# Optimization experiments

Measured on AMD Instinct MI355X. Metric: run time of the kernel, lower is better.

Reference implementation:

```python
import jax, jax.numpy as jnp
import numpy as np

B, T, HE, L, HD = 512, 512, 512, 64, 512

def setup_inputs() -> dict:
    key = jax.random.key(0)
    ks = jax.random.split(key, 16)
    def w(k, shape):
        return jax.random.normal(k, shape, dtype=jnp.float32) * 0.05
    z32 = lambda n: jnp.zeros((n,), jnp.float32)
    return {
        "input_tensor": jax.random.normal(ks[0], (B, T, 1), dtype=jnp.float32),
        # encoder LSTMCell (keras gate order i, f, g, o)
        "enc_W": w(ks[1], (1, 4 * HE)),
        "enc_U": w(ks[2], (HE, 4 * HE)),
        "enc_b": z32(4 * HE),
        # encoder mu / std heads
        "emu_W": w(ks[3], (HE, L)), "emu_b": z32(L),
        "estd_W": w(ks[4], (HE, L)), "estd_b": z32(L),
        # decoder first-state dense (tanh)
        "dfs_W": w(ks[5], (L, HD)), "dfs_b": z32(HD),
        # decoder LSTMCell
        "dec_W": w(ks[6], (L, 4 * HD)),
        "dec_U": w(ks[7], (HD, 4 * HD)),
        "dec_b": z32(4 * HD),
        # decoder mu / std heads (Dense(1))
        "dmu_W": w(ks[8], (HD, 1)), "dmu_b": z32(1),
        "dstd_W": w(ks[9], (HD, 1)), "dstd_b": z32(1),
    }

def _lstm_update(gates, c):
    i, f, g, o = jnp.split(gates, 4, axis=-1)
    c_new = jax.nn.sigmoid(f) * c + jax.nn.sigmoid(i) * jnp.tanh(g)
    h_new = jax.nn.sigmoid(o) * jnp.tanh(c_new)
    return h_new, c_new

def reference(input_tensor, enc_W, enc_U, enc_b, emu_W, emu_b, estd_W, estd_b,
              dfs_W, dfs_b, dec_W, dec_U, dec_b, dmu_W, dmu_b, dstd_W, dstd_b):
    x = input_tensor
    Bn, Tn = x.shape[0], x.shape[1]
    He = enc_U.shape[0]

    # ---- encoder: LSTM over time, keep final h ----
    def enc_step(carry, xt):
        h, c = carry
        gates = xt @ enc_W + h @ enc_U + enc_b
        return _lstm_update(gates, c), None
    h0 = jnp.zeros((Bn, He), x.dtype)
    (hT, _), _ = jax.lax.scan(enc_step, (h0, h0), jnp.swapaxes(x, 0, 1))

    mu_enc = hT @ emu_W + emu_b                       # [B, L]
    sigma_enc = jax.nn.softplus(hT @ estd_W + estd_b)  # [B, L]
    z = mu_enc  # call() uses reparam=False -> latent returns mu

    # ---- decoder: LSTM fed constant z each step ----
    hd = jnp.tanh(z @ dfs_W + dfs_b)                  # [B, HD]
    cd = jnp.zeros_like(hd)
    zin = z @ dec_W + dec_b                           # input projection constant over t
    def dec_step(carry, _):
        h, c = carry
        h_new, c_new = _lstm_update(zin + h @ dec_U, c)
        mu = h_new @ dmu_W + dmu_b                    # [B, 1]
        sg = h_new @ dstd_W + dstd_b
        return (h_new, c_new), (mu, sg)
    _, (mus, sgs) = jax.lax.scan(dec_step, (hd, cd), None, length=Tn)

    mu_dec = jnp.swapaxes(mus, 0, 1)                  # [B, T, 1]
    sigma_dec = jax.nn.softplus(jnp.swapaxes(sgs, 0, 1))
    return (mu_dec, sigma_dec, mu_enc, sigma_enc)
```

## Files before the change

### kernel.cpp

```cpp
#include <hip/hip_runtime.h>


#define B_ 512
#define T_ 512
#define H_ 512

typedef _Float16 f16;
typedef _Float16 f16x8 __attribute__((ext_vector_type(8)));
typedef float f32x16 __attribute__((ext_vector_type(16)));
typedef unsigned long long u64;
typedef unsigned int u32;

#define OFF_SG_DEC 262144
#define OFF_MU_ENC 524288
#define OFF_SG_ENC 557056

__device__ __forceinline__ float sigm_(float x) { return 1.f / (1.f + __expf(-x)); }
__device__ __forceinline__ float tanh_(float x) {
  float t = fabsf(x);
  float e = __expf(2.f * t);
  float r = 1.f - 2.f / (e + 1.f);
  return x < 0.f ? -r : r;
}
__device__ __forceinline__ float softplus_(float x) {
  return fmaxf(x, 0.f) + log1pf(__expf(-fabsf(x)));
}
__device__ __forceinline__ int fresh_(u64 w, u32 g) {
  return ((u32)(w >> 48) == g) & (((u32)(w >> 16) & 0xffffu) == g);
}
__device__ __forceinline__ u32 packh_(u64 w) {
  return (u32)(w & 0xffffu) | (((u32)(w >> 32) & 0xffffu) << 16);
}

__global__ void pack_U(const float* __restrict__ U, f16* __restrict__ Upk) {
  const int e = blockIdx.x * 256 + threadIdx.x;
  const int j = e & 7, lane = (e >> 3) & 63, ks = (e >> 9) & 31;
  const int w = (e >> 14) & 7, wg = (e >> 17) & 7;
  const int ccol = lane & 31, khalf = lane >> 5;
  const int uu = ccol >> 2, gate = ccol & 3;
  const int k = ks * 16 + khalf * 8 + j;
  const int gcol = gate * 512 + wg * 64 + w * 8 + uu;
  Upk[e] = (f16)U[k * 2048 + gcol];
}

template <int IS_DEC>
__global__ void __launch_bounds__(512, 1)
lstm_rec(const f16* __restrict__ Upk,
         const float* __restrict__ xin,
         const float* __restrict__ wa,
         const float* __restrict__ wb,
         u32* __restrict__ hbuf,
         float* __restrict__ accmu,
         float* __restrict__ accsg) {
  const int bid = blockIdx.x;
  const int s = bid >> 3;
  const int j = (bid & 7) * 4 + (s & 3);
  const int wg = s >> 2;
  const int tid = threadIdx.x, wave = tid >> 6, lane = tid & 63;
  const int U0 = wg * 64;
  const int RA = j * 16, RB = j * 16 + 8;
  const u32 GB = IS_DEC ? 0x8000u : 0u;
  const int ccol = lane & 31, khalf = lane >> 5;

  f16x8 Breg[32];
#pragma unroll
  for (int ks = 0; ks < 32; ++ks) {
    const f16* p = Upk + (((wg * 8 + wave) * 32 + ks) << 9) + lane * 8;
    asm volatile("global_load_dwordx4 %0, %1, off\n\ts_waitcnt vmcnt(0)"
                 : "=v"(Breg[ks]) : "v"(p));
  }

  const int erow = tid >> 6, eu = tid & 63;
  float xwv[4], bias[4], addA[4], addB[4];
  float dmu_w = 0.f, dstd_w = 0.f;
#pragma unroll
  for (int gt = 0; gt < 4; ++gt) {
    const int col = gt * 512 + U0 + eu;
    if (IS_DEC) {
      addA[gt] = xin[(RA + erow) * 2048 + col];
      addB[gt] = xin[(RB + erow) * 2048 + col];
      xwv[gt] = 0.f; bias[gt] = 0.f;
    } else {
      bias[gt] = wb[col];
      xwv[gt] = wa[col];
      addA[gt] = 0.f; addB[gt] = 0.f;
    }
  }
  if (IS_DEC) { dmu_w = wa[U0 + eu]; dstd_w = wb[U0 + eu]; }

  float cA = 0.f, cB = 0.f;

  __shared__ __align__(16) f16 bufA[8 * 520];
  __shared__ __align__(16) f16 bufB[8 * 520];
  __shared__ __align__(16) float gatesL[8 * 264];

  int lrow[4], lcol[4], gidxA[4], gidxB[4];
#pragma unroll
  for (int i = 0; i < 4; ++i) {
    const int w = tid + i * 512;
    lrow[i] = w >> 8; lcol[i] = w & 255;
    gidxA[i] = (RA + lrow[i]) * 256 + lcol[i];
    gidxB[i] = (RB + lrow[i]) * 256 + lcol[i];
  }
  const u64* hb64 = (const u64*)hbuf;

  u64 wAr[4], wBr[4];
#pragma unroll
  for (int i = 0; i < 4; ++i)
    wAr[i] = __hip_atomic_load(hb64 + gidxA[i], __ATOMIC_RELAXED,
                               __HIP_MEMORY_SCOPE_AGENT);
  asm volatile("" ::: "memory");

  for (int t = 0; t < T_; ++t) {
    const int b0 = (t & 1) * 131072;
    const int b1 = ((t + 1) & 1) * 131072;
    const int c1 = ((t + 1) & 1) * 262144;
    const u32 gr = GB + (u32)t, gn = GB + (u32)t + 1u;

    while (!(fresh_(wAr[0], gr) & fresh_(wAr[1], gr) &
             fresh_(wAr[2], gr) & fresh_(wAr[3], gr))) {
#pragma unroll
      for (int i = 0; i < 4; ++i)
        wAr[i] = __hip_atomic_load(hb64 + b0 + gidxA[i], __ATOMIC_RELAXED,
                                   __HIP_MEMORY_SCOPE_AGENT);
    }
#pragma unroll
    for (int i = 0; i < 4; ++i)
      *(u32*)&bufA[lrow[i] * 520 + lcol[i] * 2] = packh_(wAr[i]);
    __syncthreads();

#pragma unroll
    for (int i = 0; i < 4; ++i)
      wBr[i] = __hip_atomic_load(hb64 + b0 + gidxB[i], __ATOMIC_RELAXED,
                                 __HIP_MEMORY_SCOPE_AGENT);
    asm volatile("" ::: "memory");

    {
      f32x16 acc;
#pragma unroll
      for (int q = 0; q < 16; ++q) acc[q] = 0.f;
#pragma unroll
      for (int ks = 0; ks < 32; ++ks) {
        f16x8 a = *(const f16x8*)&bufA[(lane & 7) * 520 + ks * 16 + khalf * 8];
        acc = __builtin_amdgcn_mfma_f32_32x32x16_f16(a, Breg[ks], acc, 0, 0, 0);
      }
#pragma unroll
      for (int r = 0; r < 4; ++r)
        gatesL[(r + 4 * khalf) * 264 + wave * 32 + ccol] = acc[r];
    }
    __syncthreads();

    {
      const float4 g4 = *(const float4*)&gatesL[erow * 264 + (eu >> 3) * 32 + (eu & 7) * 4];
      float ga0, ga1, ga2, ga3;
      if (IS_DEC) {
        ga0 = g4.x + addA[0]; ga1 = g4.y + addA[1];
        ga2 = g4.z + addA[2]; ga3 = g4.w + addA[3];
      } else {
        const float xv = xin[(RA + erow) * T_ + t];
        ga0 = g4.x + bias[0] + xv * xwv[0];
        ga1 = g4.y + bias[1] + xv * xwv[1];
        ga2 = g4.z + bias[2] + xv * xwv[2];
        ga3 = g4.w + bias[3] + xv * xwv[3];
      }
      const float cn = sigm_(ga1) * cA + sigm_(ga0) * tanh_(ga2);
      cA = cn;
      const float hn = sigm_(ga3) * tanh_(cn);
      union { f16 h; unsigned short u; } hc; hc.h = (f16)hn;
      __hip_atomic_store(hbuf + c1 + (RA + erow) * 512 + U0 + eu,
                         (gn << 16) | (u32)hc.u, __ATOMIC_RELAXED,
                         __HIP_MEMORY_SCOPE_AGENT);
      if (IS_DEC) {
        float smu = hn * dmu_w, ssg = hn * dstd_w;
#pragma unroll
        for (int o = 32; o; o >>= 1) {
          smu += __shfl_xor(smu, o);
          ssg += __shfl_xor(ssg, o);
        }
        if (lane == 0) {
          unsafeAtomicAdd(&accmu[(RA + erow) * T_ + t], smu);
          unsafeAtomicAdd(&accsg[(RA + erow) * T_ + t], ssg);
        }
      }
    }

    while (!(fresh_(wBr[0], gr) & fresh_(wBr[1], gr) &
             fresh_(wBr[2], gr) & fresh_(wBr[3], gr))) {
#pragma unroll
      for (int i = 0; i < 4; ++i)
        wBr[i] = __hip_atomic_load(hb64 + b0 + gidxB[i], __ATOMIC_RELAXED,
                                   __HIP_MEMORY_SCOPE_AGENT);
    }
#pragma unroll
    for (int i = 0; i < 4; ++i)
      *(u32*)&bufB[lrow[i] * 520 + lcol[i] * 2] = packh_(wBr[i]);
    __syncthreads();

#pragma unroll
    for (int i = 0; i < 4; ++i)
      wAr[i] = __hip_atomic_load(hb64 + b1 + gidxA[i], __ATOMIC_RELAXED,
                                 __HIP_MEMORY_SCOPE_AGENT);
    asm volatile("" ::: "memory");

    {
      f32x16 acc;
#pragma unroll
      for (int q = 0; q < 16; ++q) acc[q] = 0.f;
#pragma unroll
      for (int ks = 0; ks < 32; ++ks) {
        f16x8 a = *(const f16x8*)&bufB[(lane & 7) * 520 + ks * 16 + khalf * 8];
        acc = __builtin_amdgcn_mfma_f32_32x32x16_f16(a, Breg[ks], acc, 0, 0, 0);
      }
#pragma unroll
      for (int r = 0; r < 4; ++r)
        gatesL[(r + 4 * khalf) * 264 + wave * 32 + ccol] = acc[r];
    }
    __syncthreads();

    {
      const float4 g4 = *(const float4*)&gatesL[erow * 264 + (eu >> 3) * 32 + (eu & 7) * 4];
      float ga0, ga1, ga2, ga3;
      if (IS_DEC) {
        ga0 = g4.x + addB[0]; ga1 = g4.y + addB[1];
        ga2 = g4.z + addB[2]; ga3 = g4.w + addB[3];
      } else {
        const float xv = xin[(RB + erow) * T_ + t];
        ga0 = g4.x + bias[0] + xv * xwv[0];
        ga1 = g4.y + bias[1] + xv * xwv[1];
        ga2 = g4.z + bias[2] + xv * xwv[2];
        ga3 = g4.w + bias[3] + xv * xwv[3];
      }
      const float cn = sigm_(ga1) * cB + sigm_(ga0) * tanh_(ga2);
      cB = cn;
      const float hn = sigm_(ga3) * tanh_(cn);
      union { f16 h; unsigned short u; } hc; hc.h = (f16)hn;
      __hip_atomic_store(hbuf + c1 + (RB + erow) * 512 + U0 + eu,
                         (gn << 16) | (u32)hc.u, __ATOMIC_RELAXED,
                         __HIP_MEMORY_SCOPE_AGENT);
      if (IS_DEC) {
        float smu = hn * dmu_w, ssg = hn * dstd_w;
#pragma unroll
        for (int o = 32; o; o >>= 1) {
          smu += __shfl_xor(smu, o);
          ssg += __shfl_xor(ssg, o);
        }
        if (lane == 0) {
          unsafeAtomicAdd(&accmu[(RB + erow) * T_ + t], smu);
          unsafeAtomicAdd(&accsg[(RB + erow) * T_ + t], ssg);
        }
      }
    }
  }
}

__global__ void enc_heads(const u32* __restrict__ h0, const float* __restrict__ emuW,
                          const float* __restrict__ emub, const float* __restrict__ estdW,
                          const float* __restrict__ estdb, float* __restrict__ out,
                          float* __restrict__ z) {
  const int b = blockIdx.x, tid = threadIdx.x;
  __shared__ float hrow[512];
  for (int k = tid; k < 512; k += 128) {
    union { unsigned short u; f16 h; } c;
    c.u = (unsigned short)(h0[b * 512 + k] & 0xffffu);
    hrow[k] = (float)c.h;
  }
  __syncthreads();
  const int head = tid >> 6, l = tid & 63;
  const float* W = head ? estdW : emuW;
  float a = 0.f;
#pragma unroll 8
  for (int k = 0; k < 512; ++k) a += hrow[k] * W[k * 64 + l];
  if (head == 0) {
    const float v = a + emub[l];
    out[OFF_MU_ENC + b * 64 + l] = v;
    z[b * 64 + l] = v;
  } else {
    out[OFF_SG_ENC + b * 64 + l] = softplus_(a + estdb[l]);
  }
}

__global__ void dec_prep(const float* __restrict__ z, const float* __restrict__ dfsW,
                         const float* __restrict__ dfsb, const float* __restrict__ decW,
                         const float* __restrict__ decb, u32* __restrict__ hbuf,
                         float* __restrict__ zin) {
  const int b = blockIdx.x, tid = threadIdx.x;
  __shared__ float zl[64];
  if (tid < 64) zl[tid] = z[b * 64 + tid];
  __syncthreads();
  for (int c = tid; c < 512; c += 256) {
    float a = dfsb[c];
#pragma unroll
    for (int l = 0; l < 64; ++l) a += zl[l] * dfsW[l * 512 + c];
    union { f16 h; unsigned short u; } hc; hc.h = (f16)tanh_(a);
    hbuf[b * 512 + c] = (0x8000u << 16) | (u32)hc.u;
  }
  for (int c = tid; c < 2048; c += 256) {
    float a = decb[c];
#pragma unroll
    for (int l = 0; l < 64; ++l) a += zl[l] * decW[l * 2048 + c];
    zin[b * 2048 + c] = a;
  }
}

__global__ void finalize_k(const float* __restrict__ accmu, const float* __restrict__ accsg,
                           const float* __restrict__ dmub, const float* __restrict__ dstdb,
                           float* __restrict__ out) {
  const int i = blockIdx.x * 256 + threadIdx.x;
  out[i] = accmu[i] + dmub[0];
  out[OFF_SG_DEC + i] = softplus_(accsg[i] + dstdb[0]);
}

extern "C" void kernel_launch(void* const* d_in, const int* in_sizes, int n_in,
                              void* d_out, int out_size, void* d_ws, size_t ws_size,
                              hipStream_t stream) {
  (void)in_sizes; (void)n_in; (void)out_size; (void)ws_size;
  const float* x     = (const float*)d_in[0];
  const float* encW  = (const float*)d_in[1];
  const float* encU  = (const float*)d_in[2];
  const float* encb  = (const float*)d_in[3];
  const float* emuW  = (const float*)d_in[4];
  const float* emub  = (const float*)d_in[5];
  const float* estdW = (const float*)d_in[6];
  const float* estdb = (const float*)d_in[7];
  const float* dfsW  = (const float*)d_in[8];
  const float* dfsb  = (const float*)d_in[9];
  const float* decW  = (const float*)d_in[10];
  const float* decU  = (const float*)d_in[11];
  const float* decb  = (const float*)d_in[12];
  const float* dmuW  = (const float*)d_in[13];
  const float* dmub  = (const float*)d_in[14];
  const float* dstdW = (const float*)d_in[15];
  const float* dstdb = (const float*)d_in[16];

  char* ws = (char*)d_ws;
  u32*   hbuf  = (u32*)(ws + 0);
  float* accmu = (float*)(ws + (2u << 20));
  float* accsg = (float*)(ws + (3u << 20));
  f16*   UpkE  = (f16*)(ws + (4u << 20));
  float* zin   = (float*)(ws + (4u << 20));
  f16*   UpkD  = (f16*)(ws + (8u << 20));
  float* z     = (float*)(ws + (10u << 20));
  float* out   = (float*)d_out;

  hipMemsetAsync(d_ws, 0, 4u << 20, stream);

  hipLaunchKernelGGL(pack_U, dim3(4096), dim3(256), 0, stream, encU, UpkE);
  hipLaunchKernelGGL(pack_U, dim3(4096), dim3(256), 0, stream, decU, UpkD);

  hipLaunchKernelGGL((lstm_rec<0>), dim3(256), dim3(512), 0, stream,
                     UpkE, x, encW, encb, hbuf, (float*)nullptr, (float*)nullptr);
  hipLaunchKernelGGL(enc_heads, dim3(512), dim3(128), 0, stream,
                     hbuf, emuW, emub, estdW, estdb, out, z);
  hipLaunchKernelGGL(dec_prep, dim3(512), dim3(256), 0, stream,
                     z, dfsW, dfsb, decW, decb, hbuf, zin);
  hipLaunchKernelGGL((lstm_rec<1>), dim3(256), dim3(512), 0, stream,
                     UpkD, zin, dmuW, dstdW, hbuf, accmu, accsg);
  hipLaunchKernelGGL(finalize_k, dim3(1024), dim3(256), 0, stream,
                     accmu, accsg, dmub, dstdb, out);
}
```

Before: 4.916 ms.

## Remove gate LDS round-trip via lane shuffles and compute decoder heads from staged h

The gate LDS staging buffer and its __syncthreads per half-step are replaced by in-register transposition with xor shuffles, so each lane applies the LSTM update directly on MFMA accumulator values. The decoder mu/std head dot products no longer use per-wave atomicAdds on every step. Instead, one workgroup per row group is assigned by rotation to compute them from the previous step's h already staged in LDS, with plain stores. A small tail kernel handles the final timestep, and the memset is shrunk because the accumulators are now fully overwritten. This removes barriers and atomic traffic from the serial recurrence critical path, at the cost of extra shuffles and uneven duty work across workgroups.

```diff
diff --git a/kernel.cpp b/kernel.cpp
--- a/kernel.cpp
+++ b/kernel.cpp
@@ -70,29 +70,36 @@
                  : "=v"(Breg[ks]) : "v"(p));
   }
 
-  const int erow = tid >> 6, eu = tid & 63;
-  float xwv[4], bias[4], addA[4], addB[4];
-  float dmu_w = 0.f, dstd_w = 0.f;
+  const int p_ = ccol & 3, uu_ = ccol >> 2;
+  const int row_l = p_ + 4 * khalf;
+  const int unit_l = wave * 8 + uu_;
+  float biasv[4], xwv[4], addA[4], addB[4];
 #pragma unroll
   for (int gt = 0; gt < 4; ++gt) {
-    const int col = gt * 512 + U0 + eu;
+    const int col = gt * 512 + U0 + unit_l;
     if (IS_DEC) {
-      addA[gt] = xin[(RA + erow) * 2048 + col];
-      addB[gt] = xin[(RB + erow) * 2048 + col];
-      xwv[gt] = 0.f; bias[gt] = 0.f;
+      addA[gt] = xin[(RA + row_l) * 2048 + col];
+      addB[gt] = xin[(RB + row_l) * 2048 + col];
+      biasv[gt] = 0.f; xwv[gt] = 0.f;
     } else {
-      bias[gt] = wb[col];
+      biasv[gt] = wb[col];
       xwv[gt] = wa[col];
       addA[gt] = 0.f; addB[gt] = 0.f;
     }
   }
-  if (IS_DEC) { dmu_w = wa[U0 + eu]; dstd_w = wb[U0 + eu]; }
+  float wmu[8], wsg[8];
+  if (IS_DEC) {
+#pragma unroll
+    for (int q = 0; q < 8; ++q) {
+      wmu[q] = wa[lane * 8 + q];
+      wsg[q] = wb[lane * 8 + q];
+    }
+  }
 
   float cA = 0.f, cB = 0.f;
 
   __shared__ __align__(16) f16 bufA[8 * 520];
   __shared__ __align__(16) f16 bufB[8 * 520];
-  __shared__ __align__(16) float gatesL[8 * 264];
 
   int lrow[4], lcol[4], gidxA[4], gidxB[4];
 #pragma unroll
@@ -116,6 +123,7 @@
     const int b1 = ((t + 1) & 1) * 131072;
     const int c1 = ((t + 1) & 1) * 262144;
     const u32 gr = GB + (u32)t, gn = GB + (u32)t + 1u;
+    const int duty = IS_DEC && t >= 1 && wg == (t & 7);
 
     while (!(fresh_(wAr[0], gr) & fresh_(wAr[1], gr) &
              fresh_(wAr[2], gr) & fresh_(wAr[3], gr))) {
@@ -135,7 +143,27 @@
                                  __HIP_MEMORY_SCOPE_AGENT);
     asm volatile("" ::: "memory");
 
+    if (duty) {
+      const f16x8 hv = *(const f16x8*)&bufA[wave * 520 + lane * 8];
+      float smu = 0.f, ssg = 0.f;
+#pragma unroll
+      for (int q = 0; q < 8; ++q) {
+        const float hq = (float)hv[q];
+        smu += hq * wmu[q]; ssg += hq * wsg[q];
+      }
+#pragma unroll
+      for (int o = 32; o; o >>= 1) {
+        smu += __shfl_xor(smu, o); ssg += __shfl_xor(ssg, o);
+      }
+      if (lane == 0) {
+        accmu[(RA + wave) * 512 + (t - 1)] = smu;
+        accsg[(RA + wave) * 512 + (t - 1)] = ssg;
+      }
+    }
+
     {
+      float xv = 0.f;
+      if (!IS_DEC) xv = xin[(RA + row_l) * T_ + t];
       f32x16 acc;
 #pragma unroll
       for (int q = 0; q < 16; ++q) acc[q] = 0.f;
@@ -144,44 +172,33 @@
         f16x8 a = *(const f16x8*)&bufA[(lane & 7) * 520 + ks * 16 + khalf * 8];
         acc = __builtin_amdgcn_mfma_f32_32x32x16_f16(a, Breg[ks], acc, 0, 0, 0);
       }
-#pragma unroll
-      for (int r = 0; r < 4; ++r)
-        gatesL[(r + 4 * khalf) * 264 + wave * 32 + ccol] = acc[r];
-    }
-    __syncthreads();
-
-    {
-      const float4 g4 = *(const float4*)&gatesL[erow * 264 + (eu >> 3) * 32 + (eu & 7) * 4];
+      const float x0 = acc[0], x1 = acc[1], x2 = acc[2], x3 = acc[3];
+      const int odd1 = lane & 1, odd2 = lane & 2;
+      const float t0 = __shfl_xor(x1, 1), t1 = __shfl_xor(x0, 1);
+      const float t2 = __shfl_xor(x3, 1), t3 = __shfl_xor(x2, 1);
+      const float y0 = odd1 ? t0 : x0, y1 = odd1 ? x1 : t1;
+      const float y2 = odd1 ? t2 : x2, y3 = odd1 ? x3 : t3;
+      const float s0 = __shfl_xor(y2, 2), s1 = __shfl_xor(y3, 2);
+      const float s2 = __shfl_xor(y0, 2), s3 = __shfl_xor(y1, 2);
+      const float z0 = odd2 ? s0 : y0, z1 = odd2 ? s1 : y1;
+      const float z2 = odd2 ? y2 : s2, z3 = odd2 ? y3 : s3;
       float ga0, ga1, ga2, ga3;
       if (IS_DEC) {
-        ga0 = g4.x + addA[0]; ga1 = g4.y + addA[1];
-        ga2 = g4.z + addA[2]; ga3 = g4.w + addA[3];
+        ga0 = z0 + addA[0]; ga1 = z1 + addA[1];
+        ga2 = z2 + addA[2]; ga3 = z3 + addA[3];
       } else {
-        const float xv = xin[(RA + erow) * T_ + t];
-        ga0 = g4.x + bias[0] + xv * xwv[0];
-        ga1 = g4.y + bias[1] + xv * xwv[1];
-        ga2 = g4.z + bias[2] + xv * xwv[2];
-        ga3 = g4.w + bias[3] + xv * xwv[3];
+        ga0 = z0 + biasv[0] + xv * xwv[0];
+        ga1 = z1 + biasv[1] + xv * xwv[1];
+        ga2 = z2 + biasv[2] + xv * xwv[2];
+        ga3 = z3 + biasv[3] + xv * xwv[3];
       }
       const float cn = sigm_(ga1) * cA + sigm_(ga0) * tanh_(ga2);
       cA = cn;
       const float hn = sigm_(ga3) * tanh_(cn);
       union { f16 h; unsigned short u; } hc; hc.h = (f16)hn;
-      __hip_atomic_store(hbuf + c1 + (RA + erow) * 512 + U0 + eu,
+      __hip_atomic_store(hbuf + c1 + (RA + row_l) * 512 + U0 + unit_l,
                          (gn << 16) | (u32)hc.u, __ATOMIC_RELAXED,
                          __HIP_MEMORY_SCOPE_AGENT);
-      if (IS_DEC) {
-        float smu = hn * dmu_w, ssg = hn * dstd_w;
-#pragma unroll
-        for (int o = 32; o; o >>= 1) {
-          smu += __shfl_xor(smu, o);
-          ssg += __shfl_xor(ssg, o);
-        }
-        if (lane == 0) {
-          unsafeAtomicAdd(&accmu[(RA + erow) * T_ + t], smu);
-          unsafeAtomicAdd(&accsg[(RA + erow) * T_ + t], ssg);
-        }
-      }
     }
 
     while (!(fresh_(wBr[0], gr) & fresh_(wBr[1], gr) &
@@ -202,7 +219,27 @@
                                  __HIP_MEMORY_SCOPE_AGENT);
     asm volatile("" ::: "memory");
 
+    if (duty) {
+      const f16x8 hv = *(const f16x8*)&bufB[wave * 520 + lane * 8];
+      float smu = 0.f, ssg = 0.f;
+#pragma unroll
+      for (int q = 0; q < 8; ++q) {
+        const float hq = (float)hv[q];
+        smu += hq * wmu[q]; ssg += hq * wsg[q];
+      }
+#pragma unroll
+      for (int o = 32; o; o >>= 1) {
+        smu += __shfl_xor(smu, o); ssg += __shfl_xor(ssg, o);
+      }
+      if (lane == 0) {
+        accmu[(RB + wave) * 512 + (t - 1)] = smu;
+        accsg[(RB + wave) * 512 + (t - 1)] = ssg;
+      }
+    }
+
     {
+      float xv = 0.f;
+      if (!IS_DEC) xv = xin[(RB + row_l) * T_ + t];
       f32x16 acc;
 #pragma unroll
       for (int q = 0; q < 16; ++q) acc[q] = 0.f;
@@ -211,45 +248,57 @@
         f16x8 a = *(const f16x8*)&bufB[(lane & 7) * 520 + ks * 16 + khalf * 8];
         acc = __builtin_amdgcn_mfma_f32_32x32x16_f16(a, Breg[ks], acc, 0, 0, 0);
       }
-#pragma unroll
-      for (int r = 0; r < 4; ++r)
-        gatesL[(r + 4 * khalf) * 264 + wave * 32 + ccol] = acc[r];
-    }
-    __syncthreads();
-
-    {
-      const float4 g4 = *(const float4*)&gatesL[erow * 264 + (eu >> 3) * 32 + (eu & 7) * 4];
+      const float x0 = acc[0], x1 = acc[1], x2 = acc[2], x3 = acc[3];
+      const int odd1 = lane & 1, odd2 = lane & 2;
+      const float t0 = __shfl_xor(x1, 1), t1 = __shfl_xor(x0, 1);
+      const float t2 = __shfl_xor(x3, 1), t3 = __shfl_xor(x2, 1);
+      const float y0 = odd1 ? t0 : x0, y1 = odd1 ? x1 : t1;
+      const float y2 = odd1 ? t2 : x2, y3 = odd1 ? x3 : t3;
+      const float s0 = __shfl_xor(y2, 2), s1 = __shfl_xor(y3, 2);
+      const float s2 = __shfl_xor(y0, 2), s3 = __shfl_xor(y1, 2);
+      const float z0 = odd2 ? s0 : y0, z1 = odd2 ? s1 : y1;
+      const float z2 = odd2 ? y2 : s2, z3 = odd2 ? y3 : s3;
       float ga0, ga1, ga2, ga3;
       if (IS_DEC) {
-        ga0 = g4.x + addB[0]; ga1 = g4.y + addB[1];
-        ga2 = g4.z + addB[2]; ga3 = g4.w + addB[3];
+        ga0 = z0 + addB[0]; ga1 = z1 + addB[1];
+        ga2 = z2 + addB[2]; ga3 = z3 + addB[3];
       } else {
-        const float xv = xin[(RB + erow) * T_ + t];
-        ga0 = g4.x + bias[0] + xv * xwv[0];
-        ga1 = g4.y + bias[1] + xv * xwv[1];
-        ga2 = g4.z + bias[2] + xv * xwv[2];
-        ga3 = g4.w + bias[3] + xv * xwv[3];
+        ga0 = z0 + biasv[0] + xv * xwv[0];
+        ga1 = z1 + biasv[1] + xv * xwv[1];
+        ga2 = z2 + biasv[2] + xv * xwv[2];
+        ga3 = z3 + biasv[3] + xv * xwv[3];
       }
       const float cn = sigm_(ga1) * cB + sigm_(ga0) * tanh_(ga2);
       cB = cn;
       const float hn = sigm_(ga3) * tanh_(cn);
       union { f16 h; unsigned short u; } hc; hc.h = (f16)hn;
-      __hip_atomic_store(hbuf + c1 + (RB + erow) * 512 + U0 + eu,
+      __hip_atomic_store(hbuf + c1 + (RB + row_l) * 512 + U0 + unit_l,
                          (gn << 16) | (u32)hc.u, __ATOMIC_RELAXED,
                          __HIP_MEMORY_SCOPE_AGENT);
-      if (IS_DEC) {
-        float smu = hn * dmu_w, ssg = hn * dstd_w;
-#pragma unroll
-        for (int o = 32; o; o >>= 1) {
-          smu += __shfl_xor(smu, o);
-          ssg += __shfl_xor(ssg, o);
-        }
-        if (lane == 0) {
-          unsafeAtomicAdd(&accmu[(RB + erow) * T_ + t], smu);
-          unsafeAtomicAdd(&accsg[(RB + erow) * T_ + t], ssg);
-        }
-      }
-    }
+    }
+  }
+}
+
+__global__ void dec_tail(const u32* __restrict__ hbuf, const float* __restrict__ dmuW,
+                         const float* __restrict__ dstdW, float* __restrict__ accmu,
+                         float* __restrict__ accsg) {
+  const int r = blockIdx.x, lane = threadIdx.x;
+  float smu = 0.f, ssg = 0.f;
+#pragma unroll
+  for (int q = 0; q < 8; ++q) {
+    union { unsigned short u; f16 h; } c;
+    c.u = (unsigned short)(hbuf[r * 512 + lane * 8 + q] & 0xffffu);
+    const float hq = (float)c.h;
+    smu += hq * dmuW[lane * 8 + q];
+    ssg += hq * dstdW[lane * 8 + q];
+  }
+#pragma unroll
+  for (int o = 32; o; o >>= 1) {
+    smu += __shfl_xor(smu, o); ssg += __shfl_xor(ssg, o);
+  }
+  if (lane == 0) {
+    accmu[r * 512 + 511] = smu;
+    accsg[r * 512 + 511] = ssg;
   }
 }
 
@@ -342,7 +391,7 @@
   float* z     = (float*)(ws + (10u << 20));
   float* out   = (float*)d_out;
 
-  hipMemsetAsync(d_ws, 0, 4u << 20, stream);
+  hipMemsetAsync(d_ws, 0, 2u << 20, stream);
 
   hipLaunchKernelGGL(pack_U, dim3(4096), dim3(256), 0, stream, encU, UpkE);
   hipLaunchKernelGGL(pack_U, dim3(4096), dim3(256), 0, stream, decU, UpkD);
@@ -355,6 +404,8 @@
                      z, dfsW, dfsb, decW, decb, hbuf, zin);
   hipLaunchKernelGGL((lstm_rec<1>), dim3(256), dim3(512), 0, stream,
                      UpkD, zin, dmuW, dstdW, hbuf, accmu, accsg);
+  hipLaunchKernelGGL(dec_tail, dim3(512), dim3(64), 0, stream,
+                     hbuf, dmuW, dstdW, accmu, accsg);
   hipLaunchKernelGGL(finalize_k, dim3(1024), dim3(256), 0, stream,
                      accmu, accsg, dmub, dstdb, out);
 }
```

New measurement: 5.101 ms. 3.8% more time.

## Compute decoder output heads from the gathered full h row instead of atomics

Applied to the files above, without the earlier changes.

Moves the decoder mu/std head dot products out of the gate epilogue, where each of many workgroups did partial sums and atomic adds to global accumulators. Each workgroup now computes the full dot product for its rows from the complete previous-step h row already staged in shared memory, and writes the result with plain stores lagged by one step. A small tail kernel handles the final timestep. This removes the global float atomics and lets the accumulator memset shrink. The cost is redundant head computation across the workgroups that share a row, and one extra kernel launch.

```diff
diff --git a/kernel.cpp b/kernel.cpp
--- a/kernel.cpp
+++ b/kernel.cpp
@@ -72,7 +72,6 @@
 
   const int erow = tid >> 6, eu = tid & 63;
   float xwv[4], bias[4], addA[4], addB[4];
-  float dmu_w = 0.f, dstd_w = 0.f;
 #pragma unroll
   for (int gt = 0; gt < 4; ++gt) {
     const int col = gt * 512 + U0 + eu;
@@ -86,7 +85,14 @@
       addA[gt] = 0.f; addB[gt] = 0.f;
     }
   }
-  if (IS_DEC) { dmu_w = wa[U0 + eu]; dstd_w = wb[U0 + eu]; }
+  float wmu[8], wsg[8];
+  if (IS_DEC) {
+#pragma unroll
+    for (int q = 0; q < 8; ++q) {
+      wmu[q] = wa[lane * 8 + q];
+      wsg[q] = wb[lane * 8 + q];
+    }
+  }
 
   float cA = 0.f, cB = 0.f;
 
@@ -134,6 +140,24 @@
       wBr[i] = __hip_atomic_load(hb64 + b0 + gidxB[i], __ATOMIC_RELAXED,
                                  __HIP_MEMORY_SCOPE_AGENT);
     asm volatile("" ::: "memory");
+
+    if (IS_DEC && t >= 1) {
+      const f16x8 hv = *(const f16x8*)&bufA[wave * 520 + lane * 8];
+      float smu = 0.f, ssg = 0.f;
+#pragma unroll
+      for (int q = 0; q < 8; ++q) {
+        const float hq = (float)hv[q];
+        smu += hq * wmu[q]; ssg += hq * wsg[q];
+      }
+#pragma unroll
+      for (int o = 32; o; o >>= 1) {
+        smu += __shfl_xor(smu, o); ssg += __shfl_xor(ssg, o);
+      }
+      if (lane == 0) {
+        accmu[(RA + wave) * 512 + (t - 1)] = smu;
+        accsg[(RA + wave) * 512 + (t - 1)] = ssg;
+      }
+    }
 
     {
       f32x16 acc;
@@ -170,18 +194,6 @@
       __hip_atomic_store(hbuf + c1 + (RA + erow) * 512 + U0 + eu,
                          (gn << 16) | (u32)hc.u, __ATOMIC_RELAXED,
                          __HIP_MEMORY_SCOPE_AGENT);
-      if (IS_DEC) {
-        float smu = hn * dmu_w, ssg = hn * dstd_w;
-#pragma unroll
-        for (int o = 32; o; o >>= 1) {
-          smu += __shfl_xor(smu, o);
-          ssg += __shfl_xor(ssg, o);
-        }
-        if (lane == 0) {
-          unsafeAtomicAdd(&accmu[(RA + erow) * T_ + t], smu);
-          unsafeAtomicAdd(&accsg[(RA + erow) * T_ + t], ssg);
-        }
-      }
     }
 
     while (!(fresh_(wBr[0], gr) & fresh_(wBr[1], gr) &
@@ -201,6 +213,24 @@
       wAr[i] = __hip_atomic_load(hb64 + b1 + gidxA[i], __ATOMIC_RELAXED,
                                  __HIP_MEMORY_SCOPE_AGENT);
     asm volatile("" ::: "memory");
+
+    if (IS_DEC && t >= 1) {
+      const f16x8 hv = *(const f16x8*)&bufB[wave * 520 + lane * 8];
+      float smu = 0.f, ssg = 0.f;
+#pragma unroll
+      for (int q = 0; q < 8; ++q) {
+        const float hq = (float)hv[q];
+        smu += hq * wmu[q]; ssg += hq * wsg[q];
+      }
+#pragma unroll
+      for (int o = 32; o; o >>= 1) {
+        smu += __shfl_xor(smu, o); ssg += __shfl_xor(ssg, o);
+      }
+      if (lane == 0) {
+        accmu[(RB + wave) * 512 + (t - 1)] = smu;
+        accsg[(RB + wave) * 512 + (t - 1)] = ssg;
+      }
+    }
 
     {
       f32x16 acc;
@@ -237,19 +267,30 @@
       __hip_atomic_store(hbuf + c1 + (RB + erow) * 512 + U0 + eu,
                          (gn << 16) | (u32)hc.u, __ATOMIC_RELAXED,
                          __HIP_MEMORY_SCOPE_AGENT);
-      if (IS_DEC) {
-        float smu = hn * dmu_w, ssg = hn * dstd_w;
-#pragma unroll
-        for (int o = 32; o; o >>= 1) {
-          smu += __shfl_xor(smu, o);
-          ssg += __shfl_xor(ssg, o);
-        }
-        if (lane == 0) {
-          unsafeAtomicAdd(&accmu[(RB + erow) * T_ + t], smu);
-          unsafeAtomicAdd(&accsg[(RB + erow) * T_ + t], ssg);
-        }
-      }
-    }
+    }
+  }
+}
+
+__global__ void dec_tail(const u32* __restrict__ hbuf, const float* __restrict__ dmuW,
+                         const float* __restrict__ dstdW, float* __restrict__ accmu,
+                         float* __restrict__ accsg) {
+  const int r = blockIdx.x, lane = threadIdx.x;
+  float smu = 0.f, ssg = 0.f;
+#pragma unroll
+  for (int q = 0; q < 8; ++q) {
+    union { unsigned short u; f16 h; } c;
+    c.u = (unsigned short)(hbuf[r * 512 + lane * 8 + q] & 0xffffu);
+    const float hq = (float)c.h;
+    smu += hq * dmuW[lane * 8 + q];
+    ssg += hq * dstdW[lane * 8 + q];
+  }
+#pragma unroll
+  for (int o = 32; o; o >>= 1) {
+    smu += __shfl_xor(smu, o); ssg += __shfl_xor(ssg, o);
+  }
+  if (lane == 0) {
+    accmu[r * 512 + 511] = smu;
+    accsg[r * 512 + 511] = ssg;
   }
 }
 
@@ -342,7 +383,7 @@
   float* z     = (float*)(ws + (10u << 20));
   float* out   = (float*)d_out;
 
-  hipMemsetAsync(d_ws, 0, 4u << 20, stream);
+  hipMemsetAsync(d_ws, 0, 2u << 20, stream);
 
   hipLaunchKernelGGL(pack_U, dim3(4096), dim3(256), 0, stream, encU, UpkE);
   hipLaunchKernelGGL(pack_U, dim3(4096), dim3(256), 0, stream, decU, UpkD);
@@ -355,6 +396,8 @@
                      z, dfsW, dfsb, decW, decb, hbuf, zin);
   hipLaunchKernelGGL((lstm_rec<1>), dim3(256), dim3(512), 0, stream,
                      UpkD, zin, dmuW, dstdW, hbuf, accmu, accsg);
+  hipLaunchKernelGGL(dec_tail, dim3(512), dim3(64), 0, stream,
+                     hbuf, dmuW, dstdW, accmu, accsg);
   hipLaunchKernelGGL(finalize_k, dim3(1024), dim3(256), 0, stream,
                      accmu, accsg, dmub, dstdb, out);
 }
```

New measurement: 4.999 ms. About the same (+1.7%).
